# Kernel tuning notes

Measured on AMD Instinct MI355X. Metric: run time of the kernel, lower is better.

The kernel has to match this reference:

```python
import jax, jax.numpy as jnp
import numpy as np

HIDDEN = 1024
TILE = 128


def setup_inputs() -> dict:
    key = jax.random.key(0)
    ks = jax.random.split(key, 9)
    B, S, D = 2, 4096, HIDDEN
    s = 1.0 / np.sqrt(D)
    return {
        "batch": jax.random.normal(ks[0], (B, S, D), jnp.float32),
        "Wq": jax.random.normal(ks[1], (D, D), jnp.float32) * s,
        "bq": jax.random.normal(ks[2], (D,), jnp.float32) * 0.01,
        "Wk": jax.random.normal(ks[3], (D, D), jnp.float32) * s,
        "bk": jax.random.normal(ks[4], (D,), jnp.float32) * 0.01,
        "Wv": jax.random.normal(ks[5], (D, D), jnp.float32) * s,
        "bv": jax.random.normal(ks[6], (D,), jnp.float32) * 0.01,
        "Wo": jax.random.normal(ks[7], (D, D), jnp.float32) * s,
        "bo": jax.random.normal(ks[8], (D,), jnp.float32) * 0.01,
    }


def reference(batch, Wq, bq, Wk, bk, Wv, bv, Wo, bo):
    B, S, D = batch.shape
    scale = 1.0 / np.sqrt(D)
    T = S // TILE  # seq_len chosen divisible by tile size

    # Projections (nn.Linear: x @ W.T + b)
    q = batch @ Wq.T + bq
    k = batch @ Wk.T + bk
    v = batch @ Wv.T + bv

    # Tile K/V along the sequence axis: [B, T, TILE, D]
    k_t = k.reshape(B, T, TILE, D)
    v_t = v.reshape(B, T, TILE, D)

    # Per-tile scores and per-tile softmax (NOT a global softmax —
    # faithful to the module, which normalizes within each kv tile).
    scores = jnp.einsum("bqd,btkd->btqk", q, k_t) * scale  # [B, T, S, TILE]
    w = jax.nn.softmax(scores, axis=-1)

    # Sum of per-tile attention outputs over kv tiles
    out = jnp.einsum("btqk,btkd->bqd", w, v_t)  # [B, S, D]

    # Normalizing factor: sum of per-tile softmax weights (== T analytically,
    # computed explicitly to match the original math bit-for-bit in spirit)
    norm = w.sum(axis=-1).sum(axis=1)[..., None]  # [B, S, 1]
    out = out / (norm + 1e-6)

    return out @ Wo.T + bo
```

## Files before the change

kernel.cpp:

```cpp
#include <hip/hip_runtime.h>


#define D_ 1024
#define S_ 4096
#define B_ 2

typedef unsigned short u16;
typedef float f32x4 __attribute__((ext_vector_type(4)));
typedef float float4v __attribute__((ext_vector_type(4)));
typedef __bf16 bf16x8 __attribute__((ext_vector_type(8)));
typedef unsigned short us8 __attribute__((ext_vector_type(8)));

static __device__ __forceinline__ u16 f2bf(float f) {
    unsigned int u = __builtin_bit_cast(unsigned int, f);
    u += 0x7FFFu + ((u >> 16) & 1u);
    return (u16)(u >> 16);
}

static __device__ __forceinline__ void gld16(const u16* g, u16* l) {
    __builtin_amdgcn_global_load_lds(
        (const __attribute__((address_space(1))) void*)g,
        (__attribute__((address_space(3))) void*)l, 16, 0, 0);
}

template <int N>
static __device__ __forceinline__ void waitv() {
    if constexpr (N == 0)      asm volatile("s_waitcnt vmcnt(0)" ::: "memory");
    else if constexpr (N == 3) asm volatile("s_waitcnt vmcnt(3)" ::: "memory");
    else if constexpr (N == 4) asm volatile("s_waitcnt vmcnt(4)" ::: "memory");
    else if constexpr (N == 6) asm volatile("s_waitcnt vmcnt(6)" ::: "memory");
    else if constexpr (N == 8) asm volatile("s_waitcnt vmcnt(8)" ::: "memory");
}

static __device__ __forceinline__ void xcd_map(int& bx, int& by) {
    const int gx = gridDim.x, gy = gridDim.y;
    int lin = blockIdx.x + blockIdx.y * gx;
    int ry = gy >> 3;
    int idx = lin >> 3;
    int q = idx / ry;
    bx = q;
    by = (lin & 7) * ry + (idx - q * ry);
}

__global__ void cast_kernel(const float* __restrict__ in, u16* __restrict__ out, int n8) {
    int i = blockIdx.x * blockDim.x + threadIdx.x;
    int stride = gridDim.x * blockDim.x;
    for (; i < n8; i += stride) {
        const float4v* p = (const float4v*)in + 2 * (size_t)i;
        float4v a = p[0], b = p[1];
        us8 o;
        o[0] = f2bf(a[0]); o[1] = f2bf(a[1]); o[2] = f2bf(a[2]); o[3] = f2bf(a[3]);
        o[4] = f2bf(b[0]); o[5] = f2bf(b[1]); o[6] = f2bf(b[2]); o[7] = f2bf(b[3]);
        *((us8*)out + i) = o;
    }
}

__global__ void cast4_kernel(const float* __restrict__ w0, const float* __restrict__ w1,
                             const float* __restrict__ w2, const float* __restrict__ w3,
                             u16* __restrict__ out, int n8per) {
    const float* srcs[4] = {w0, w1, w2, w3};
    const float* in = srcs[blockIdx.y];
    u16* o = out + (size_t)blockIdx.y * (size_t)n8per * 8;
    int i = blockIdx.x * blockDim.x + threadIdx.x;
    int stride = gridDim.x * blockDim.x;
    for (; i < n8per; i += stride) {
        const float4v* p = (const float4v*)in + 2 * (size_t)i;
        float4v a = p[0], b = p[1];
        us8 v;
        v[0] = f2bf(a[0]); v[1] = f2bf(a[1]); v[2] = f2bf(a[2]); v[3] = f2bf(a[3]);
        v[4] = f2bf(b[0]); v[5] = f2bf(b[1]); v[6] = f2bf(b[2]); v[7] = f2bf(b[3]);
        *((us8*)o + i) = v;
    }
}

__global__ void concat_bias(const float* __restrict__ b0, const float* __restrict__ b1,
                            const float* __restrict__ b2, float* __restrict__ out) {
    int i = blockIdx.x * 256 + threadIdx.x;
    const float* s = (i < 1024) ? b0 : ((i < 2048) ? b1 : b2);
    out[i] = s[i & 1023];
}

__global__ void transpose_v(const u16* __restrict__ V, u16* __restrict__ Vt, int ldv) {
    __shared__ u16 t[64][72];
    const int tid = threadIdx.x;
    const int d0 = blockIdx.x * 64;
    const int s0 = blockIdx.y * 64;
    const u16* Vb = V + (size_t)blockIdx.z * ((size_t)S_ * ldv);
    u16* Vtb = Vt + (size_t)blockIdx.z * ((size_t)D_ * S_);
#pragma unroll
    for (int it = 0; it < 2; it++) {
        int idx = it * 256 + tid;
        int row = idx >> 3;
        int ch = idx & 7;
        us8 v = *(const us8*)&Vb[(size_t)(s0 + row) * ldv + d0 + ch * 8];
        *(us8*)&t[row][ch * 8] = v;
    }
    __syncthreads();
#pragma unroll
    for (int it = 0; it < 2; it++) {
        int idx = it * 256 + tid;
        int jj = idx >> 3;
        int ch = idx & 7;
        us8 v;
#pragma unroll
        for (int e = 0; e < 8; e++) v[e] = t[ch * 8 + e][jj];
        *(us8*)&Vtb[(size_t)(d0 + jj) * S_ + s0 + ch * 8] = v;
    }
}

template <int BM, int EPI>
__global__ __launch_bounds__(512, 1) void gemm8(
    const u16* __restrict__ A, const u16* __restrict__ B, void* __restrict__ Cv,
    const float* __restrict__ bias, int K, int lda, int ldb, int ldc,
    long sA, long sB, long sC, float scale)
{
    constexpr int MI = BM / 32;
    constexpr int MH = MI / 2;
    constexpr int LPT_A = BM / 128;
    constexpr int LPT = LPT_A + 2;

    __shared__ u16 lA[4][BM * 32];
    __shared__ u16 lB[4][256 * 32];
    __shared__ float sred[2][8][128];

    const int tid = threadIdx.x;
    const int lane = tid & 63;
    const int wid = tid >> 6;
    const int wr = wid >> 2;
    const int wc = wid & 3;
    const int ar = lane & 15;
    const int sl = lane >> 4;
    const int z = blockIdx.z;
    A += (size_t)z * sA;
    B += (size_t)z * sB;
    int bx, by;
    xcd_map(bx, by);
    const int m0 = by * BM;
    const int n0 = bx * 256;
    const int NT = K >> 5;

    f32x4 acc[MI][4];
#pragma unroll
    for (int i = 0; i < MI; i++)
#pragma unroll
        for (int j = 0; j < 4; j++)
#pragma unroll
            for (int r = 0; r < 4; r++) acc[i][j][r] = 0.0f;

    auto stageA = [&](int t) {
        const int k0 = t << 5;
        u16* dst = &lA[t & 3][0];
#pragma unroll
        for (int j = 0; j < LPT_A; j++) {
            int u = wid * (BM >> 1) + j * 64 + lane;
            int row = u >> 2, ps = u & 3;
            int ls = ps ^ ((row >> 1) & 3);
            gld16(A + (size_t)(m0 + row) * lda + k0 + ls * 8, dst + u * 8);
        }
    };
    auto stageB = [&](int t) {
        const int k0 = t << 5;
        u16* dst = &lB[t & 3][0];
#pragma unroll
        for (int j = 0; j < 2; j++) {
            int u = wid * 128 + j * 64 + lane;
            int row = u >> 2, ps = u & 3;
            int ls = ps ^ ((row >> 1) & 3);
            gld16(B + (size_t)(n0 + row) * ldb + k0 + ls * 8, dst + u * 8);
        }
    };
    auto rdA = [&](int buf, int mi) -> bf16x8 {
        int R = wr * (BM / 2) + mi * 16 + ar;
        int ps = sl ^ ((R >> 1) & 3);
        return *(const bf16x8*)&lA[buf][R * 32 + ps * 8];
    };
    auto rdB = [&](int buf, int ni) -> bf16x8 {
        int R = wc * 64 + ni * 16 + ar;
        int ps = sl ^ ((R >> 1) & 3);
        return *(const bf16x8*)&lB[buf][R * 32 + ps * 8];
    };

    stageA(0); stageB(0);
    stageA(1); stageB(1);
    stageA(2); stageB(2);

    for (int t = 0; t < NT; ++t) {
        const int ahead = NT - 1 - t;
        if (ahead >= 2)      waitv<2 * LPT>();
        else if (ahead == 1) waitv<LPT>();
        else                 waitv<0>();
        __builtin_amdgcn_s_barrier();

        const int buf = t & 3;
        bf16x8 bfr[4];
#pragma unroll
        for (int ni = 0; ni < 4; ni++) bfr[ni] = rdB(buf, ni);
        bf16x8 afr[MH];
#pragma unroll
        for (int mi = 0; mi < MH; mi++) afr[mi] = rdA(buf, mi);
        if (t + 3 < NT) stageA(t + 3);
        asm volatile("s_waitcnt lgkmcnt(0)" ::: "memory");
        __builtin_amdgcn_sched_barrier(0);
        __builtin_amdgcn_s_setprio(1);
#pragma unroll
        for (int mi = 0; mi < MH; mi++)
#pragma unroll
            for (int ni = 0; ni < 4; ni++)
                acc[mi][ni] = __builtin_amdgcn_mfma_f32_16x16x32_bf16(
                    afr[mi], bfr[ni], acc[mi][ni], 0, 0, 0);
        __builtin_amdgcn_s_setprio(0);
        __builtin_amdgcn_s_barrier();

        bf16x8 afr2[MH];
#pragma unroll
        for (int mi = 0; mi < MH; mi++) afr2[mi] = rdA(buf, MH + mi);
        if (t + 3 < NT) stageB(t + 3);
        asm volatile("s_waitcnt lgkmcnt(0)" ::: "memory");
        __builtin_amdgcn_sched_barrier(0);
        __builtin_amdgcn_s_setprio(1);
#pragma unroll
        for (int mi = 0; mi < MH; mi++)
#pragma unroll
            for (int ni = 0; ni < 4; ni++)
                acc[MH + mi][ni] = __builtin_amdgcn_mfma_f32_16x16x32_bf16(
                    afr2[mi], bfr[ni], acc[MH + mi][ni], 0, 0, 0);
        __builtin_amdgcn_s_setprio(0);
    }

    if constexpr (EPI == 3) {
        const float SL = 0.03125f * 1.44269504088896341f;
#pragma unroll
        for (int mi = 0; mi < MI; mi++) {
#pragma unroll
            for (int r = 0; r < 4; r++) {
                float m = acc[mi][0][r];
#pragma unroll
                for (int ni = 1; ni < 4; ni++) m = fmaxf(m, acc[mi][ni][r]);
                m = fmaxf(m, __shfl_xor(m, 1));
                m = fmaxf(m, __shfl_xor(m, 2));
                m = fmaxf(m, __shfl_xor(m, 4));
                m = fmaxf(m, __shfl_xor(m, 8));
                if (ar == 0) sred[0][wid][mi * 16 + sl * 4 + r] = m;
            }
        }
        __syncthreads();
#pragma unroll
        for (int mi = 0; mi < MI; mi++) {
#pragma unroll
            for (int r = 0; r < 4; r++) {
                const int rl = mi * 16 + sl * 4 + r;
                const float mc = fmaxf(sred[0][wid][rl], sred[0][wid ^ 1][rl]);
                float s = 0.0f;
#pragma unroll
                for (int ni = 0; ni < 4; ni++) {
                    float e = exp2f((acc[mi][ni][r] - mc) * SL);
                    acc[mi][ni][r] = e;
                    s += e;
                }
                s += __shfl_xor(s, 1);
                s += __shfl_xor(s, 2);
                s += __shfl_xor(s, 4);
                s += __shfl_xor(s, 8);
                if (ar == 0) sred[1][wid][rl] = s;
            }
        }
        __syncthreads();
        u16* C = (u16*)Cv + (size_t)z * sC;
#pragma unroll
        for (int mi = 0; mi < MI; mi++) {
#pragma unroll
            for (int r = 0; r < 4; r++) {
                const int rl = mi * 16 + sl * 4 + r;
                const float inv = 1.0f / (sred[1][wid][rl] + sred[1][wid ^ 1][rl]);
                const int row = m0 + wr * (BM / 2) + rl;
#pragma unroll
                for (int ni = 0; ni < 4; ni++)
                    C[(size_t)row * ldc + n0 + wc * 64 + ni * 16 + ar] =
                        f2bf(acc[mi][ni][r] * inv);
            }
        }
    } else {
#pragma unroll
        for (int mi = 0; mi < MI; mi++) {
#pragma unroll
            for (int ni = 0; ni < 4; ni++) {
                const int col = n0 + wc * 64 + ni * 16 + ar;
                const int rowb = m0 + wr * (BM / 2) + mi * 16 + sl * 4;
                if constexpr (EPI == 0) {
                    u16* C = (u16*)Cv + (size_t)z * sC;
                    const float bv = bias[col];
#pragma unroll
                    for (int r = 0; r < 4; r++)
                        C[(size_t)(rowb + r) * ldc + col] = f2bf(acc[mi][ni][r] + bv);
                } else if constexpr (EPI == 1) {
                    u16* C = (u16*)Cv + (size_t)z * sC;
#pragma unroll
                    for (int r = 0; r < 4; r++)
                        C[(size_t)(rowb + r) * ldc + col] = f2bf(acc[mi][ni][r] * scale);
                } else {
                    float* C = (float*)Cv + (size_t)z * sC;
                    const float bv = bias[col];
#pragma unroll
                    for (int r = 0; r < 4; r++)
                        C[(size_t)(rowb + r) * ldc + col] = acc[mi][ni][r] + bv;
                }
            }
        }
    }
}

extern "C" void kernel_launch(void* const* d_in, const int* in_sizes, int n_in,
                              void* d_out, int out_size, void* d_ws, size_t ws_size,
                              hipStream_t stream)
{
    const float* X  = (const float*)d_in[0];
    const float* Wq = (const float*)d_in[1];
    const float* bq = (const float*)d_in[2];
    const float* Wk = (const float*)d_in[3];
    const float* bk = (const float*)d_in[4];
    const float* Wv = (const float*)d_in[5];
    const float* bv = (const float*)d_in[6];
    const float* Wo = (const float*)d_in[7];
    const float* bo = (const float*)d_in[8];
    float* OUT = (float*)d_out;

    u16* ws = (u16*)d_ws;
    const size_t NTOK = (size_t)B_ * S_;
    const size_t XSZ = NTOK * D_;
    u16* Xb   = ws;
    u16* QKVb = Xb + XSZ;
    u16* Vt   = QKVb + NTOK * (size_t)(3 * D_);
    u16* Wqb  = Vt + XSZ;
    u16* Wsm  = Wqb + (size_t)4 * D_ * D_;
    float* bqkv = (float*)(Wsm + (size_t)B_ * S_ * S_);
    u16* Ob   = Xb;

    u16* Qp = QKVb;
    u16* Kp = QKVb + D_;
    u16* Vp = QKVb + 2 * D_;
    const int ldqkv = 3 * D_;

    cast_kernel<<<dim3(2048), dim3(256), 0, stream>>>(X, Xb, (int)(XSZ / 8));
    cast4_kernel<<<dim3(512, 4), dim3(256), 0, stream>>>(Wq, Wk, Wv, Wo, Wqb,
                                                         (int)((size_t)D_ * D_ / 8));
    concat_bias<<<dim3(12), dim3(256), 0, stream>>>(bq, bk, bv, bqkv);

    gemm8<128, 0><<<dim3(3 * D_ / 256, NTOK / 128, 1), 512, 0, stream>>>(
        Xb, Wqb, QKVb, bqkv, D_, D_, D_, ldqkv, 0, 0, 0, 1.0f);

    transpose_v<<<dim3(D_ / 64, S_ / 64, B_), 256, 0, stream>>>(Vp, Vt, ldqkv);

    gemm8<256, 3><<<dim3(S_ / 256, S_ / 256, B_), 512, 0, stream>>>(
        Qp, Kp, Wsm, nullptr, D_, ldqkv, ldqkv, S_,
        (long)S_ * ldqkv, (long)S_ * ldqkv, (long)S_ * S_, 1.0f);

    gemm8<128, 1><<<dim3(D_ / 256, S_ / 128, B_), 512, 0, stream>>>(
        Wsm, Vt, Ob, nullptr, S_, S_, S_, D_,
        (long)S_ * S_, (long)D_ * S_, (long)S_ * D_, 1.0f / (32.0f + 1e-6f));

    gemm8<128, 2><<<dim3(D_ / 256, NTOK / 128, 1), 512, 0, stream>>>(
        Ob, Wqb + (size_t)3 * D_ * D_, OUT, bo, D_, D_, D_, D_, 0, 0, 0, 1.0f);
}
```

Measured before the change: 406.4 us.

## Rewrite GEMM mainloops with 64-wide K tiles and finer-grained load/MFMA interleaving

Replaces the templated gemm8 kernel with two specialized kernels. Both use a K-step of 64 in place of 32, with an XOR swizzle over 8 chunks. The 256x256 softmax GEMM now double-buffers with global loads split into half-tile pieces interleaved between quarter-tile MFMA phases. The 128-row GEMM uses a 3-stage ring buffer with two MFMA phases per K-step. The aim is fewer barriers and waitcnts per unit of work and better overlap of global-to-LDS copies with matrix math, at the cost of larger LDS footprint and more complex synchronization.

```diff
diff --git a/kernel.cpp b/kernel.cpp
--- a/kernel.cpp
+++ b/kernel.cpp
@@ -26,10 +26,13 @@
 template <int N>
 static __device__ __forceinline__ void waitv() {
     if constexpr (N == 0)      asm volatile("s_waitcnt vmcnt(0)" ::: "memory");
-    else if constexpr (N == 3) asm volatile("s_waitcnt vmcnt(3)" ::: "memory");
-    else if constexpr (N == 4) asm volatile("s_waitcnt vmcnt(4)" ::: "memory");
+    else if constexpr (N == 2) asm volatile("s_waitcnt vmcnt(2)" ::: "memory");
     else if constexpr (N == 6) asm volatile("s_waitcnt vmcnt(6)" ::: "memory");
-    else if constexpr (N == 8) asm volatile("s_waitcnt vmcnt(8)" ::: "memory");
+}
+
+static __device__ __forceinline__ void lgkm0sb() {
+    asm volatile("s_waitcnt lgkmcnt(0)" ::: "memory");
+    __builtin_amdgcn_sched_barrier(0);
 }
 
 static __device__ __forceinline__ void xcd_map(int& bx, int& by) {
@@ -108,202 +111,340 @@
     }
 }
 
-template <int BM, int EPI>
-__global__ __launch_bounds__(512, 1) void gemm8(
-    const u16* __restrict__ A, const u16* __restrict__ B, void* __restrict__ Cv,
-    const float* __restrict__ bias, int K, int lda, int ldb, int ldc,
-    long sA, long sB, long sC, float scale)
+#define MMQ(ACC, MB, NB)                                                      \
+    {                                                                         \
+        _Pragma("unroll") for (int mi_ = 0; mi_ < 4; ++mi_) {                 \
+            _Pragma("unroll") for (int ni_ = 0; ni_ < 2; ++ni_) {             \
+                _Pragma("unroll") for (int kh_ = 0; kh_ < 2; ++kh_) {         \
+                    ACC[(MB) + mi_][(NB) + ni_] =                             \
+                        __builtin_amdgcn_mfma_f32_16x16x32_bf16(              \
+                            af[mi_][kh_], bf[ni_][kh_],                       \
+                            ACC[(MB) + mi_][(NB) + ni_], 0, 0, 0);            \
+                }                                                             \
+            }                                                                 \
+        }                                                                     \
+    }
+
+__global__ __launch_bounds__(512, 1) void gemm_sm256(
+    const u16* __restrict__ A, const u16* __restrict__ B, u16* __restrict__ C,
+    int K, int lda, int ldb, int ldc, long sA, long sB, long sC)
 {
-    constexpr int MI = BM / 32;
-    constexpr int MH = MI / 2;
-    constexpr int LPT_A = BM / 128;
-    constexpr int LPT = LPT_A + 2;
-
-    __shared__ u16 lA[4][BM * 32];
-    __shared__ u16 lB[4][256 * 32];
+    __shared__ u16 lA[2][256 * 64];
+    __shared__ u16 lB[2][256 * 64];
     __shared__ float sred[2][8][128];
-
-    const int tid = threadIdx.x;
-    const int lane = tid & 63;
-    const int wid = tid >> 6;
-    const int wr = wid >> 2;
-    const int wc = wid & 3;
-    const int ar = lane & 15;
-    const int sl = lane >> 4;
+    const int tid = threadIdx.x, lane = tid & 63, wid = tid >> 6;
+    const int wr = wid >> 2, wc = wid & 3;
+    const int ar = lane & 15, sl = lane >> 4;
     const int z = blockIdx.z;
     A += (size_t)z * sA;
     B += (size_t)z * sB;
     int bx, by;
     xcd_map(bx, by);
-    const int m0 = by * BM;
-    const int n0 = bx * 256;
-    const int NT = K >> 5;
-
-    f32x4 acc[MI][4];
-#pragma unroll
-    for (int i = 0; i < MI; i++)
+    const int m0 = by * 256, n0 = bx * 256;
+    const int NT = K >> 6, NI = NT >> 1;
+
+    f32x4 acc[8][4];
+#pragma unroll
+    for (int i = 0; i < 8; i++)
 #pragma unroll
         for (int j = 0; j < 4; j++)
 #pragma unroll
             for (int r = 0; r < 4; r++) acc[i][j][r] = 0.0f;
 
-    auto stageA = [&](int t) {
-        const int k0 = t << 5;
-        u16* dst = &lA[t & 3][0];
-#pragma unroll
-        for (int j = 0; j < LPT_A; j++) {
-            int u = wid * (BM >> 1) + j * 64 + lane;
-            int row = u >> 2, ps = u & 3;
-            int ls = ps ^ ((row >> 1) & 3);
-            gld16(A + (size_t)(m0 + row) * lda + k0 + ls * 8, dst + u * 8);
+    auto stg = [&](const u16* __restrict__ M, int ld, int mb, u16* ld0, int t, int h) {
+#pragma unroll
+        for (int j = 0; j < 2; ++j) {
+            const int u = j * 512 + wid * 64 + lane;
+            const int row = h * 128 + (u >> 3);
+            const int ls = (u & 7) ^ (row & 7);
+            gld16(M + (size_t)(mb + row) * ld + (t << 6) + ls * 8, ld0 + h * 8192 + u * 8);
         }
     };
-    auto stageB = [&](int t) {
-        const int k0 = t << 5;
-        u16* dst = &lB[t & 3][0];
-#pragma unroll
-        for (int j = 0; j < 2; j++) {
-            int u = wid * 128 + j * 64 + lane;
-            int row = u >> 2, ps = u & 3;
-            int ls = ps ^ ((row >> 1) & 3);
-            gld16(B + (size_t)(n0 + row) * ldb + k0 + ls * 8, dst + u * 8);
-        }
+    auto rd = [&](const u16* l, int R, int kh) -> bf16x8 {
+        const int ps = ((kh << 2) | sl) ^ (R & 7);
+        return *(const bf16x8*)&l[R * 64 + ps * 8];
     };
-    auto rdA = [&](int buf, int mi) -> bf16x8 {
-        int R = wr * (BM / 2) + mi * 16 + ar;
-        int ps = sl ^ ((R >> 1) & 3);
-        return *(const bf16x8*)&lA[buf][R * 32 + ps * 8];
+
+    stg(A, lda, m0, lA[0], 0, 0); stg(A, lda, m0, lA[0], 0, 1);
+    stg(B, ldb, n0, lB[0], 0, 0); stg(B, ldb, n0, lB[0], 0, 1);
+    stg(A, lda, m0, lA[1], 1, 0);
+    waitv<2>();
+    __builtin_amdgcn_s_barrier();
+
+    bf16x8 af[4][2], bf[2][2];
+    for (int j = 0; j < NI; ++j) {
+        const int a = 2 * j, b = a + 1;
+        const bool s2 = (j + 1 < NI);
+#pragma unroll
+        for (int mi = 0; mi < 4; ++mi)
+#pragma unroll
+            for (int kh = 0; kh < 2; ++kh)
+                af[mi][kh] = rd(lA[0], wr * 128 + mi * 16 + ar, kh);
+#pragma unroll
+        for (int ni = 0; ni < 2; ++ni)
+#pragma unroll
+            for (int kh = 0; kh < 2; ++kh)
+                bf[ni][kh] = rd(lB[0], wc * 64 + ni * 16 + ar, kh);
+        stg(A, lda, m0, lA[1], b, 1);
+        lgkm0sb();
+        __builtin_amdgcn_s_setprio(1);
+        MMQ(acc, 0, 0);
+        __builtin_amdgcn_s_setprio(0);
+        __builtin_amdgcn_s_barrier();
+#pragma unroll
+        for (int ni = 0; ni < 2; ++ni)
+#pragma unroll
+            for (int kh = 0; kh < 2; ++kh)
+                bf[ni][kh] = rd(lB[0], wc * 64 + (2 + ni) * 16 + ar, kh);
+        stg(B, ldb, n0, lB[1], b, 0);
+        lgkm0sb();
+        __builtin_amdgcn_s_setprio(1);
+        MMQ(acc, 0, 2);
+        __builtin_amdgcn_s_setprio(0);
+        __builtin_amdgcn_s_barrier();
+#pragma unroll
+        for (int mi = 0; mi < 4; ++mi)
+#pragma unroll
+            for (int kh = 0; kh < 2; ++kh)
+                af[mi][kh] = rd(lA[0], wr * 128 + (4 + mi) * 16 + ar, kh);
+        stg(B, ldb, n0, lB[1], b, 1);
+        lgkm0sb();
+        __builtin_amdgcn_s_setprio(1);
+        MMQ(acc, 4, 2);
+        __builtin_amdgcn_s_setprio(0);
+        __builtin_amdgcn_s_barrier();
+#pragma unroll
+        for (int ni = 0; ni < 2; ++ni)
+#pragma unroll
+            for (int kh = 0; kh < 2; ++kh)
+                bf[ni][kh] = rd(lB[0], wc * 64 + ni * 16 + ar, kh);
+        if (s2) stg(A, lda, m0, lA[0], a + 2, 0);
+        lgkm0sb();
+        __builtin_amdgcn_s_setprio(1);
+        MMQ(acc, 4, 0);
+        __builtin_amdgcn_s_setprio(0);
+        if (s2) waitv<2>(); else waitv<0>();
+        __builtin_amdgcn_s_barrier();
+#pragma unroll
+        for (int mi = 0; mi < 4; ++mi)
+#pragma unroll
+            for (int kh = 0; kh < 2; ++kh)
+                af[mi][kh] = rd(lA[1], wr * 128 + mi * 16 + ar, kh);
+#pragma unroll
+        for (int ni = 0; ni < 2; ++ni)
+#pragma unroll
+            for (int kh = 0; kh < 2; ++kh)
+                bf[ni][kh] = rd(lB[1], wc * 64 + ni * 16 + ar, kh);
+        if (s2) stg(B, ldb, n0, lB[0], a + 2, 0);
+        lgkm0sb();
+        __builtin_amdgcn_s_setprio(1);
+        MMQ(acc, 0, 0);
+        __builtin_amdgcn_s_setprio(0);
+        __builtin_amdgcn_s_barrier();
+#pragma unroll
+        for (int ni = 0; ni < 2; ++ni)
+#pragma unroll
+            for (int kh = 0; kh < 2; ++kh)
+                bf[ni][kh] = rd(lB[1], wc * 64 + (2 + ni) * 16 + ar, kh);
+        if (s2) stg(B, ldb, n0, lB[0], a + 2, 1);
+        lgkm0sb();
+        __builtin_amdgcn_s_setprio(1);
+        MMQ(acc, 0, 2);
+        __builtin_amdgcn_s_setprio(0);
+        __builtin_amdgcn_s_barrier();
+#pragma unroll
+        for (int mi = 0; mi < 4; ++mi)
+#pragma unroll
+            for (int kh = 0; kh < 2; ++kh)
+                af[mi][kh] = rd(lA[1], wr * 128 + (4 + mi) * 16 + ar, kh);
+        if (s2) stg(A, lda, m0, lA[0], a + 2, 1);
+        lgkm0sb();
+        __builtin_amdgcn_s_setprio(1);
+        MMQ(acc, 4, 2);
+        __builtin_amdgcn_s_setprio(0);
+        __builtin_amdgcn_s_barrier();
+#pragma unroll
+        for (int ni = 0; ni < 2; ++ni)
+#pragma unroll
+            for (int kh = 0; kh < 2; ++kh)
+                bf[ni][kh] = rd(lB[1], wc * 64 + ni * 16 + ar, kh);
+        if (s2) stg(A, lda, m0, lA[1], b + 2, 0);
+        lgkm0sb();
+        __builtin_amdgcn_s_setprio(1);
+        MMQ(acc, 4, 0);
+        __builtin_amdgcn_s_setprio(0);
+        if (s2) waitv<2>(); else waitv<0>();
+        __builtin_amdgcn_s_barrier();
+    }
+
+    const float SL = 0.03125f * 1.44269504088896341f;
+#pragma unroll
+    for (int mi = 0; mi < 8; mi++) {
+#pragma unroll
+        for (int r = 0; r < 4; r++) {
+            float m = acc[mi][0][r];
+#pragma unroll
+            for (int ni = 1; ni < 4; ni++) m = fmaxf(m, acc[mi][ni][r]);
+            m = fmaxf(m, __shfl_xor(m, 1));
+            m = fmaxf(m, __shfl_xor(m, 2));
+            m = fmaxf(m, __shfl_xor(m, 4));
+            m = fmaxf(m, __shfl_xor(m, 8));
+            if (ar == 0) sred[0][wid][mi * 16 + sl * 4 + r] = m;
+        }
+    }
+    __syncthreads();
+#pragma unroll
+    for (int mi = 0; mi < 8; mi++) {
+#pragma unroll
+        for (int r = 0; r < 4; r++) {
+            const int rl = mi * 16 + sl * 4 + r;
+            const float mc = fmaxf(sred[0][wid][rl], sred[0][wid ^ 1][rl]);
+            float s = 0.0f;
+#pragma unroll
+            for (int ni = 0; ni < 4; ni++) {
+                float e = exp2f((acc[mi][ni][r] - mc) * SL);
+                acc[mi][ni][r] = e;
+                s += e;
+            }
+            s += __shfl_xor(s, 1);
+            s += __shfl_xor(s, 2);
+            s += __shfl_xor(s, 4);
+            s += __shfl_xor(s, 8);
+            if (ar == 0) sred[1][wid][rl] = s;
+        }
+    }
+    __syncthreads();
+    u16* Cp = C + (size_t)z * sC;
+#pragma unroll
+    for (int mi = 0; mi < 8; mi++) {
+#pragma unroll
+        for (int r = 0; r < 4; r++) {
+            const int rl = mi * 16 + sl * 4 + r;
+            const float inv = 1.0f / (sred[1][wid][rl] + sred[1][wid ^ 1][rl]);
+            const int row = m0 + wr * 128 + rl;
+#pragma unroll
+            for (int ni = 0; ni < 4; ni++)
+                Cp[(size_t)row * ldc + n0 + wc * 64 + ni * 16 + ar] =
+                    f2bf(acc[mi][ni][r] * inv);
+        }
+    }
+}
+
+template <int EPI>
+__global__ __launch_bounds__(512, 1) void gemm128(
+    const u16* __restrict__ A, const u16* __restrict__ B, void* __restrict__ Cv,
+    const float* __restrict__ bias, int K, int lda, int ldb, int ldc,
+    long sA, long sB, long sC, float scale)
+{
+    __shared__ u16 lA[3][128 * 64];
+    __shared__ u16 lB[3][256 * 64];
+    const int tid = threadIdx.x, lane = tid & 63, wid = tid >> 6;
+    const int wr = wid >> 2, wc = wid & 3;
+    const int ar = lane & 15, sl = lane >> 4;
+    const int z = blockIdx.z;
+    A += (size_t)z * sA;
+    B += (size_t)z * sB;
+    int bx, by;
+    xcd_map(bx, by);
+    const int m0 = by * 128, n0 = bx * 256;
+    const int NT = K >> 6;
+
+    f32x4 acc[4][4];
+#pragma unroll
+    for (int i = 0; i < 4; i++)
+#pragma unroll
+        for (int j = 0; j < 4; j++)
+#pragma unroll
+            for (int r = 0; r < 4; r++) acc[i][j][r] = 0.0f;
+
+    auto stgA = [&](int t) {
+        u16* dst = &lA[t % 3][0];
+#pragma unroll
+        for (int j = 0; j < 2; ++j) {
+            const int u = j * 512 + wid * 64 + lane;
+            const int row = u >> 3;
+            const int ls = (u & 7) ^ (row & 7);
+            gld16(A + (size_t)(m0 + row) * lda + (t << 6) + ls * 8, dst + u * 8);
+        }
     };
-    auto rdB = [&](int buf, int ni) -> bf16x8 {
-        int R = wc * 64 + ni * 16 + ar;
-        int ps = sl ^ ((R >> 1) & 3);
-        return *(const bf16x8*)&lB[buf][R * 32 + ps * 8];
+    auto stgB = [&](int t, int h) {
+        u16* dst = &lB[t % 3][0];
+#pragma unroll
+        for (int j = 0; j < 2; ++j) {
+            const int u = j * 512 + wid * 64 + lane;
+            const int row = h * 128 + (u >> 3);
+            const int ls = (u & 7) ^ (row & 7);
+            gld16(B + (size_t)(n0 + row) * ldb + (t << 6) + ls * 8, dst + h * 8192 + u * 8);
+        }
     };
-
-    stageA(0); stageB(0);
-    stageA(1); stageB(1);
-    stageA(2); stageB(2);
-
+    auto rd = [&](const u16* l, int R, int kh) -> bf16x8 {
+        const int ps = ((kh << 2) | sl) ^ (R & 7);
+        return *(const bf16x8*)&l[R * 64 + ps * 8];
+    };
+
+    stgA(0); stgB(0, 0); stgB(0, 1);
+    stgA(1); stgB(1, 0); stgB(1, 1);
+    waitv<6>();
+    __builtin_amdgcn_s_barrier();
+
+    bf16x8 af[4][2], bf[2][2];
     for (int t = 0; t < NT; ++t) {
-        const int ahead = NT - 1 - t;
-        if (ahead >= 2)      waitv<2 * LPT>();
-        else if (ahead == 1) waitv<LPT>();
-        else                 waitv<0>();
-        __builtin_amdgcn_s_barrier();
-
-        const int buf = t & 3;
-        bf16x8 bfr[4];
-#pragma unroll
-        for (int ni = 0; ni < 4; ni++) bfr[ni] = rdB(buf, ni);
-        bf16x8 afr[MH];
-#pragma unroll
-        for (int mi = 0; mi < MH; mi++) afr[mi] = rdA(buf, mi);
-        if (t + 3 < NT) stageA(t + 3);
-        asm volatile("s_waitcnt lgkmcnt(0)" ::: "memory");
-        __builtin_amdgcn_sched_barrier(0);
-        __builtin_amdgcn_s_setprio(1);
-#pragma unroll
-        for (int mi = 0; mi < MH; mi++)
-#pragma unroll
-            for (int ni = 0; ni < 4; ni++)
-                acc[mi][ni] = __builtin_amdgcn_mfma_f32_16x16x32_bf16(
-                    afr[mi], bfr[ni], acc[mi][ni], 0, 0, 0);
-        __builtin_amdgcn_s_setprio(0);
-        __builtin_amdgcn_s_barrier();
-
-        bf16x8 afr2[MH];
-#pragma unroll
-        for (int mi = 0; mi < MH; mi++) afr2[mi] = rdA(buf, MH + mi);
-        if (t + 3 < NT) stageB(t + 3);
-        asm volatile("s_waitcnt lgkmcnt(0)" ::: "memory");
-        __builtin_amdgcn_sched_barrier(0);
-        __builtin_amdgcn_s_setprio(1);
-#pragma unroll
-        for (int mi = 0; mi < MH; mi++)
-#pragma unroll
-            for (int ni = 0; ni < 4; ni++)
-                acc[MH + mi][ni] = __builtin_amdgcn_mfma_f32_16x16x32_bf16(
-                    afr2[mi], bfr[ni], acc[MH + mi][ni], 0, 0, 0);
-        __builtin_amdgcn_s_setprio(0);
-    }
-
-    if constexpr (EPI == 3) {
-        const float SL = 0.03125f * 1.44269504088896341f;
-#pragma unroll
-        for (int mi = 0; mi < MI; mi++) {
-#pragma unroll
-            for (int r = 0; r < 4; r++) {
-                float m = acc[mi][0][r];
-#pragma unroll
-                for (int ni = 1; ni < 4; ni++) m = fmaxf(m, acc[mi][ni][r]);
-                m = fmaxf(m, __shfl_xor(m, 1));
-                m = fmaxf(m, __shfl_xor(m, 2));
-                m = fmaxf(m, __shfl_xor(m, 4));
-                m = fmaxf(m, __shfl_xor(m, 8));
-                if (ar == 0) sred[0][wid][mi * 16 + sl * 4 + r] = m;
-            }
-        }
-        __syncthreads();
-#pragma unroll
-        for (int mi = 0; mi < MI; mi++) {
-#pragma unroll
-            for (int r = 0; r < 4; r++) {
-                const int rl = mi * 16 + sl * 4 + r;
-                const float mc = fmaxf(sred[0][wid][rl], sred[0][wid ^ 1][rl]);
-                float s = 0.0f;
-#pragma unroll
-                for (int ni = 0; ni < 4; ni++) {
-                    float e = exp2f((acc[mi][ni][r] - mc) * SL);
-                    acc[mi][ni][r] = e;
-                    s += e;
-                }
-                s += __shfl_xor(s, 1);
-                s += __shfl_xor(s, 2);
-                s += __shfl_xor(s, 4);
-                s += __shfl_xor(s, 8);
-                if (ar == 0) sred[1][wid][rl] = s;
-            }
-        }
-        __syncthreads();
-        u16* C = (u16*)Cv + (size_t)z * sC;
-#pragma unroll
-        for (int mi = 0; mi < MI; mi++) {
-#pragma unroll
-            for (int r = 0; r < 4; r++) {
-                const int rl = mi * 16 + sl * 4 + r;
-                const float inv = 1.0f / (sred[1][wid][rl] + sred[1][wid ^ 1][rl]);
-                const int row = m0 + wr * (BM / 2) + rl;
-#pragma unroll
-                for (int ni = 0; ni < 4; ni++)
-                    C[(size_t)row * ldc + n0 + wc * 64 + ni * 16 + ar] =
-                        f2bf(acc[mi][ni][r] * inv);
-            }
-        }
-    } else {
-#pragma unroll
-        for (int mi = 0; mi < MI; mi++) {
-#pragma unroll
-            for (int ni = 0; ni < 4; ni++) {
-                const int col = n0 + wc * 64 + ni * 16 + ar;
-                const int rowb = m0 + wr * (BM / 2) + mi * 16 + sl * 4;
-                if constexpr (EPI == 0) {
-                    u16* C = (u16*)Cv + (size_t)z * sC;
-                    const float bv = bias[col];
-#pragma unroll
-                    for (int r = 0; r < 4; r++)
-                        C[(size_t)(rowb + r) * ldc + col] = f2bf(acc[mi][ni][r] + bv);
-                } else if constexpr (EPI == 1) {
-                    u16* C = (u16*)Cv + (size_t)z * sC;
-#pragma unroll
-                    for (int r = 0; r < 4; r++)
-                        C[(size_t)(rowb + r) * ldc + col] = f2bf(acc[mi][ni][r] * scale);
-                } else {
-                    float* C = (float*)Cv + (size_t)z * sC;
-                    const float bv = bias[col];
-#pragma unroll
-                    for (int r = 0; r < 4; r++)
-                        C[(size_t)(rowb + r) * ldc + col] = acc[mi][ni][r] + bv;
-                }
+        const u16* bufA = &lA[t % 3][0];
+        const u16* bufB = &lB[t % 3][0];
+        const bool s2 = (t + 2 < NT);
+#pragma unroll
+        for (int mi = 0; mi < 4; ++mi)
+#pragma unroll
+            for (int kh = 0; kh < 2; ++kh)
+                af[mi][kh] = rd(bufA, wr * 64 + mi * 16 + ar, kh);
+#pragma unroll
+        for (int ni = 0; ni < 2; ++ni)
+#pragma unroll
+            for (int kh = 0; kh < 2; ++kh)
+                bf[ni][kh] = rd(bufB, wc * 64 + ni * 16 + ar, kh);
+        if (s2) { stgA(t + 2); stgB(t + 2, 0); }
+        lgkm0sb();
+        __builtin_amdgcn_s_setprio(1);
+        MMQ(acc, 0, 0);
+        __builtin_amdgcn_s_setprio(0);
+        __builtin_amdgcn_s_barrier();
+#pragma unroll
+        for (int ni = 0; ni < 2; ++ni)
+#pragma unroll
+            for (int kh = 0; kh < 2; ++kh)
+                bf[ni][kh] = rd(bufB, wc * 64 + (2 + ni) * 16 + ar, kh);
+        if (s2) stgB(t + 2, 1);
+        lgkm0sb();
+        __builtin_amdgcn_s_setprio(1);
+        MMQ(acc, 0, 2);
+        __builtin_amdgcn_s_setprio(0);
+        if (s2) waitv<6>(); else waitv<0>();
+        __builtin_amdgcn_s_barrier();
+    }
+
+#pragma unroll
+    for (int mi = 0; mi < 4; mi++) {
+#pragma unroll
+        for (int ni = 0; ni < 4; ni++) {
+            const int col = n0 + wc * 64 + ni * 16 + ar;
+            const int rowb = m0 + wr * 64 + mi * 16 + sl * 4;
+            if constexpr (EPI == 0) {
+                u16* C = (u16*)Cv + (size_t)z * sC;
+                const float bv = bias[col];
+#pragma unroll
+                for (int r = 0; r < 4; r++)
+                    C[(size_t)(rowb + r) * ldc + col] = f2bf(acc[mi][ni][r] + bv);
+            } else if constexpr (EPI == 1) {
+                u16* C = (u16*)Cv + (size_t)z * sC;
+#pragma unroll
+                for (int r = 0; r < 4; r++)
+                    C[(size_t)(rowb + r) * ldc + col] = f2bf(acc[mi][ni][r] * scale);
+            } else {
+                float* C = (float*)Cv + (size_t)z * sC;
+                const float bv = bias[col];
+#pragma unroll
+                for (int r = 0; r < 4; r++)
+                    C[(size_t)(rowb + r) * ldc + col] = acc[mi][ni][r] + bv;
             }
         }
     }
@@ -345,19 +486,19 @@
                                                          (int)((size_t)D_ * D_ / 8));
     concat_bias<<<dim3(12), dim3(256), 0, stream>>>(bq, bk, bv, bqkv);
 
-    gemm8<128, 0><<<dim3(3 * D_ / 256, NTOK / 128, 1), 512, 0, stream>>>(
+    gemm128<0><<<dim3(3 * D_ / 256, NTOK / 128, 1), 512, 0, stream>>>(
         Xb, Wqb, QKVb, bqkv, D_, D_, D_, ldqkv, 0, 0, 0, 1.0f);
 
     transpose_v<<<dim3(D_ / 64, S_ / 64, B_), 256, 0, stream>>>(Vp, Vt, ldqkv);
 
-    gemm8<256, 3><<<dim3(S_ / 256, S_ / 256, B_), 512, 0, stream>>>(
-        Qp, Kp, Wsm, nullptr, D_, ldqkv, ldqkv, S_,
-        (long)S_ * ldqkv, (long)S_ * ldqkv, (long)S_ * S_, 1.0f);
-
-    gemm8<128, 1><<<dim3(D_ / 256, S_ / 128, B_), 512, 0, stream>>>(
+    gemm_sm256<<<dim3(S_ / 256, S_ / 256, B_), 512, 0, stream>>>(
+        Qp, Kp, Wsm, D_, ldqkv, ldqkv, S_,
+        (long)S_ * ldqkv, (long)S_ * ldqkv, (long)S_ * S_);
+
+    gemm128<1><<<dim3(D_ / 256, S_ / 128, B_), 512, 0, stream>>>(
         Wsm, Vt, Ob, nullptr, S_, S_, S_, D_,
         (long)S_ * S_, (long)D_ * S_, (long)S_ * D_, 1.0f / (32.0f + 1e-6f));
 
-    gemm8<128, 2><<<dim3(D_ / 256, NTOK / 128, 1), 512, 0, stream>>>(
+    gemm128<2><<<dim3(D_ / 256, NTOK / 128, 1), 512, 0, stream>>>(
         Ob, Wqb + (size_t)3 * D_ * D_, OUT, bo, D_, D_, D_, D_, 0, 0, 0, 1.0f);
 }
```

Result: faster. 372.7 us (-8.3%).

## Rewrite GEMM with BK=64 triple-buffered pipeline and fixed 128x256 tiles

Applied to the files above, without the earlier changes.

Replaces the templated BM GEMM, which used a K-step of 32 with four LDS buffers, with a fixed 128x256 tile GEMM that uses a K-step of 64, three LDS buffers and an 8-way XOR swizzle. Each iteration now issues twice as many MFMAs per barrier, split into two N-halves, and the B tile is staged in two halves to interleave the loads with compute. The QK^T scores GEMM moves from 256x256 to 128x256 tiles, which doubles its grid and changes reuse. The aim is to halve the barrier and wait overhead per unit of K. The cost is more LDS use and a shallower prefetch distance, two K-steps ahead instead of three.

```diff
diff --git a/kernel.cpp b/kernel.cpp
--- a/kernel.cpp
+++ b/kernel.cpp
@@ -26,10 +26,12 @@
 template <int N>
 static __device__ __forceinline__ void waitv() {
     if constexpr (N == 0)      asm volatile("s_waitcnt vmcnt(0)" ::: "memory");
-    else if constexpr (N == 3) asm volatile("s_waitcnt vmcnt(3)" ::: "memory");
-    else if constexpr (N == 4) asm volatile("s_waitcnt vmcnt(4)" ::: "memory");
     else if constexpr (N == 6) asm volatile("s_waitcnt vmcnt(6)" ::: "memory");
-    else if constexpr (N == 8) asm volatile("s_waitcnt vmcnt(8)" ::: "memory");
+}
+
+static __device__ __forceinline__ void lgkm0sb() {
+    asm volatile("s_waitcnt lgkmcnt(0)" ::: "memory");
+    __builtin_amdgcn_sched_barrier(0);
 }
 
 static __device__ __forceinline__ void xcd_map(int& bx, int& by) {
@@ -108,129 +110,117 @@
     }
 }
 
-template <int BM, int EPI>
-__global__ __launch_bounds__(512, 1) void gemm8(
+#define MMQ(ACC, MB, NB)                                                      \
+    {                                                                         \
+        _Pragma("unroll") for (int mi_ = 0; mi_ < 4; ++mi_) {                 \
+            _Pragma("unroll") for (int ni_ = 0; ni_ < 2; ++ni_) {             \
+                _Pragma("unroll") for (int kh_ = 0; kh_ < 2; ++kh_) {         \
+                    ACC[(MB) + mi_][(NB) + ni_] =                             \
+                        __builtin_amdgcn_mfma_f32_16x16x32_bf16(              \
+                            af[mi_][kh_], bf[ni_][kh_],                       \
+                            ACC[(MB) + mi_][(NB) + ni_], 0, 0, 0);            \
+                }                                                             \
+            }                                                                 \
+        }                                                                     \
+    }
+
+template <int EPI>
+__global__ __launch_bounds__(512, 1) void gemm128(
     const u16* __restrict__ A, const u16* __restrict__ B, void* __restrict__ Cv,
     const float* __restrict__ bias, int K, int lda, int ldb, int ldc,
     long sA, long sB, long sC, float scale)
 {
-    constexpr int MI = BM / 32;
-    constexpr int MH = MI / 2;
-    constexpr int LPT_A = BM / 128;
-    constexpr int LPT = LPT_A + 2;
-
-    __shared__ u16 lA[4][BM * 32];
-    __shared__ u16 lB[4][256 * 32];
-    __shared__ float sred[2][8][128];
-
-    const int tid = threadIdx.x;
-    const int lane = tid & 63;
-    const int wid = tid >> 6;
-    const int wr = wid >> 2;
-    const int wc = wid & 3;
-    const int ar = lane & 15;
-    const int sl = lane >> 4;
+    __shared__ u16 lA[3][128 * 64];
+    __shared__ u16 lB[3][256 * 64];
+    __shared__ float sred[2][8][64];
+    const int tid = threadIdx.x, lane = tid & 63, wid = tid >> 6;
+    const int wr = wid >> 2, wc = wid & 3;
+    const int ar = lane & 15, sl = lane >> 4;
     const int z = blockIdx.z;
     A += (size_t)z * sA;
     B += (size_t)z * sB;
     int bx, by;
     xcd_map(bx, by);
-    const int m0 = by * BM;
-    const int n0 = bx * 256;
-    const int NT = K >> 5;
-
-    f32x4 acc[MI][4];
-#pragma unroll
-    for (int i = 0; i < MI; i++)
+    const int m0 = by * 128, n0 = bx * 256;
+    const int NT = K >> 6;
+
+    f32x4 acc[4][4];
+#pragma unroll
+    for (int i = 0; i < 4; i++)
 #pragma unroll
         for (int j = 0; j < 4; j++)
 #pragma unroll
             for (int r = 0; r < 4; r++) acc[i][j][r] = 0.0f;
 
-    auto stageA = [&](int t) {
-        const int k0 = t << 5;
-        u16* dst = &lA[t & 3][0];
-#pragma unroll
-        for (int j = 0; j < LPT_A; j++) {
-            int u = wid * (BM >> 1) + j * 64 + lane;
-            int row = u >> 2, ps = u & 3;
-            int ls = ps ^ ((row >> 1) & 3);
-            gld16(A + (size_t)(m0 + row) * lda + k0 + ls * 8, dst + u * 8);
+    auto stgA = [&](int t) {
+        u16* dst = &lA[t % 3][0];
+#pragma unroll
+        for (int j = 0; j < 2; ++j) {
+            const int u = j * 512 + wid * 64 + lane;
+            const int row = u >> 3;
+            const int ls = (u & 7) ^ (row & 7);
+            gld16(A + (size_t)(m0 + row) * lda + (t << 6) + ls * 8, dst + u * 8);
         }
     };
-    auto stageB = [&](int t) {
-        const int k0 = t << 5;
-        u16* dst = &lB[t & 3][0];
-#pragma unroll
-        for (int j = 0; j < 2; j++) {
-            int u = wid * 128 + j * 64 + lane;
-            int row = u >> 2, ps = u & 3;
-            int ls = ps ^ ((row >> 1) & 3);
-            gld16(B + (size_t)(n0 + row) * ldb + k0 + ls * 8, dst + u * 8);
+    auto stgB = [&](int t, int h) {
+        u16* dst = &lB[t % 3][0];
+#pragma unroll
+        for (int j = 0; j < 2; ++j) {
+            const int u = j * 512 + wid * 64 + lane;
+            const int row = h * 128 + (u >> 3);
+            const int ls = (u & 7) ^ (row & 7);
+            gld16(B + (size_t)(n0 + row) * ldb + (t << 6) + ls * 8, dst + h * 8192 + u * 8);
         }
     };
-    auto rdA = [&](int buf, int mi) -> bf16x8 {
-        int R = wr * (BM / 2) + mi * 16 + ar;
-        int ps = sl ^ ((R >> 1) & 3);
-        return *(const bf16x8*)&lA[buf][R * 32 + ps * 8];
+    auto rd = [&](const u16* l, int R, int kh) -> bf16x8 {
+        const int ps = ((kh << 2) | sl) ^ (R & 7);
+        return *(const bf16x8*)&l[R * 64 + ps * 8];
     };
-    auto rdB = [&](int buf, int ni) -> bf16x8 {
-        int R = wc * 64 + ni * 16 + ar;
-        int ps = sl ^ ((R >> 1) & 3);
-        return *(const bf16x8*)&lB[buf][R * 32 + ps * 8];
-    };
-
-    stageA(0); stageB(0);
-    stageA(1); stageB(1);
-    stageA(2); stageB(2);
-
+
+    stgA(0); stgB(0, 0); stgB(0, 1);
+    stgA(1); stgB(1, 0); stgB(1, 1);
+    waitv<6>();
+    __builtin_amdgcn_s_barrier();
+
+    bf16x8 af[4][2], bf[2][2];
     for (int t = 0; t < NT; ++t) {
-        const int ahead = NT - 1 - t;
-        if (ahead >= 2)      waitv<2 * LPT>();
-        else if (ahead == 1) waitv<LPT>();
-        else                 waitv<0>();
-        __builtin_amdgcn_s_barrier();
-
-        const int buf = t & 3;
-        bf16x8 bfr[4];
-#pragma unroll
-        for (int ni = 0; ni < 4; ni++) bfr[ni] = rdB(buf, ni);
-        bf16x8 afr[MH];
-#pragma unroll
-        for (int mi = 0; mi < MH; mi++) afr[mi] = rdA(buf, mi);
-        if (t + 3 < NT) stageA(t + 3);
-        asm volatile("s_waitcnt lgkmcnt(0)" ::: "memory");
-        __builtin_amdgcn_sched_barrier(0);
+        const u16* bufA = &lA[t % 3][0];
+        const u16* bufB = &lB[t % 3][0];
+        const bool s2 = (t + 2 < NT);
+#pragma unroll
+        for (int mi = 0; mi < 4; ++mi)
+#pragma unroll
+            for (int kh = 0; kh < 2; ++kh)
+                af[mi][kh] = rd(bufA, wr * 64 + mi * 16 + ar, kh);
+#pragma unroll
+        for (int ni = 0; ni < 2; ++ni)
+#pragma unroll
+            for (int kh = 0; kh < 2; ++kh)
+                bf[ni][kh] = rd(bufB, wc * 64 + ni * 16 + ar, kh);
+        if (s2) { stgA(t + 2); stgB(t + 2, 0); }
+        lgkm0sb();
         __builtin_amdgcn_s_setprio(1);
-#pragma unroll
-        for (int mi = 0; mi < MH; mi++)
-#pragma unroll
-            for (int ni = 0; ni < 4; ni++)
-                acc[mi][ni] = __builtin_amdgcn_mfma_f32_16x16x32_bf16(
-                    afr[mi], bfr[ni], acc[mi][ni], 0, 0, 0);
+        MMQ(acc, 0, 0);
         __builtin_amdgcn_s_setprio(0);
         __builtin_amdgcn_s_barrier();
-
-        bf16x8 afr2[MH];
-#pragma unroll
-        for (int mi = 0; mi < MH; mi++) afr2[mi] = rdA(buf, MH + mi);
-        if (t + 3 < NT) stageB(t + 3);
-        asm volatile("s_waitcnt lgkmcnt(0)" ::: "memory");
-        __builtin_amdgcn_sched_barrier(0);
+#pragma unroll
+        for (int ni = 0; ni < 2; ++ni)
+#pragma unroll
+            for (int kh = 0; kh < 2; ++kh)
+                bf[ni][kh] = rd(bufB, wc * 64 + (2 + ni) * 16 + ar, kh);
+        if (s2) stgB(t + 2, 1);
+        lgkm0sb();
         __builtin_amdgcn_s_setprio(1);
-#pragma unroll
-        for (int mi = 0; mi < MH; mi++)
-#pragma unroll
-            for (int ni = 0; ni < 4; ni++)
-                acc[MH + mi][ni] = __builtin_amdgcn_mfma_f32_16x16x32_bf16(
-                    afr2[mi], bfr[ni], acc[MH + mi][ni], 0, 0, 0);
+        MMQ(acc, 0, 2);
         __builtin_amdgcn_s_setprio(0);
+        if (s2) waitv<6>(); else waitv<0>();
+        __builtin_amdgcn_s_barrier();
     }
 
     if constexpr (EPI == 3) {
         const float SL = 0.03125f * 1.44269504088896341f;
 #pragma unroll
-        for (int mi = 0; mi < MI; mi++) {
+        for (int mi = 0; mi < 4; mi++) {
 #pragma unroll
             for (int r = 0; r < 4; r++) {
                 float m = acc[mi][0][r];
@@ -245,7 +235,7 @@
         }
         __syncthreads();
 #pragma unroll
-        for (int mi = 0; mi < MI; mi++) {
+        for (int mi = 0; mi < 4; mi++) {
 #pragma unroll
             for (int r = 0; r < 4; r++) {
                 const int rl = mi * 16 + sl * 4 + r;
@@ -267,12 +257,12 @@
         __syncthreads();
         u16* C = (u16*)Cv + (size_t)z * sC;
 #pragma unroll
-        for (int mi = 0; mi < MI; mi++) {
+        for (int mi = 0; mi < 4; mi++) {
 #pragma unroll
             for (int r = 0; r < 4; r++) {
                 const int rl = mi * 16 + sl * 4 + r;
                 const float inv = 1.0f / (sred[1][wid][rl] + sred[1][wid ^ 1][rl]);
-                const int row = m0 + wr * (BM / 2) + rl;
+                const int row = m0 + wr * 64 + rl;
 #pragma unroll
                 for (int ni = 0; ni < 4; ni++)
                     C[(size_t)row * ldc + n0 + wc * 64 + ni * 16 + ar] =
@@ -281,11 +271,11 @@
         }
     } else {
 #pragma unroll
-        for (int mi = 0; mi < MI; mi++) {
+        for (int mi = 0; mi < 4; mi++) {
 #pragma unroll
             for (int ni = 0; ni < 4; ni++) {
                 const int col = n0 + wc * 64 + ni * 16 + ar;
-                const int rowb = m0 + wr * (BM / 2) + mi * 16 + sl * 4;
+                const int rowb = m0 + wr * 64 + mi * 16 + sl * 4;
                 if constexpr (EPI == 0) {
                     u16* C = (u16*)Cv + (size_t)z * sC;
                     const float bv = bias[col];
@@ -345,19 +335,19 @@
                                                          (int)((size_t)D_ * D_ / 8));
     concat_bias<<<dim3(12), dim3(256), 0, stream>>>(bq, bk, bv, bqkv);
 
-    gemm8<128, 0><<<dim3(3 * D_ / 256, NTOK / 128, 1), 512, 0, stream>>>(
+    gemm128<0><<<dim3(3 * D_ / 256, NTOK / 128, 1), 512, 0, stream>>>(
         Xb, Wqb, QKVb, bqkv, D_, D_, D_, ldqkv, 0, 0, 0, 1.0f);
 
     transpose_v<<<dim3(D_ / 64, S_ / 64, B_), 256, 0, stream>>>(Vp, Vt, ldqkv);
 
-    gemm8<256, 3><<<dim3(S_ / 256, S_ / 256, B_), 512, 0, stream>>>(
+    gemm128<3><<<dim3(S_ / 256, S_ / 128, B_), 512, 0, stream>>>(
         Qp, Kp, Wsm, nullptr, D_, ldqkv, ldqkv, S_,
         (long)S_ * ldqkv, (long)S_ * ldqkv, (long)S_ * S_, 1.0f);
 
-    gemm8<128, 1><<<dim3(D_ / 256, S_ / 128, B_), 512, 0, stream>>>(
+    gemm128<1><<<dim3(D_ / 256, S_ / 128, B_), 512, 0, stream>>>(
         Wsm, Vt, Ob, nullptr, S_, S_, S_, D_,
         (long)S_ * S_, (long)D_ * S_, (long)S_ * D_, 1.0f / (32.0f + 1e-6f));
 
-    gemm8<128, 2><<<dim3(D_ / 256, NTOK / 128, 1), 512, 0, stream>>>(
+    gemm128<2><<<dim3(D_ / 256, NTOK / 128, 1), 512, 0, stream>>>(
         Ob, Wqb + (size_t)3 * D_ * D_, OUT, bo, D_, D_, D_, D_, 0, 0, 0, 1.0f);
 }
```

Result: faster. 386.0 us (-5.0%).
